# Kernel optimization log

Hardware: AMD Instinct MI355X
Metric: run time of the kernel (lower is better)

## Reference

```python
import jax, jax.numpy as jnp
import numpy as np

B, T, C, H = 4, 2048, 768, 12
HD = C // H  # 64
EPS = 1e-5


def layer_norm(x, g, b):
    mu = jnp.mean(x, axis=-1, keepdims=True)
    var = jnp.var(x, axis=-1, keepdims=True)
    return (x - mu) * jax.lax.rsqrt(var + EPS) * g + b


def setup_inputs() -> dict:
    key = jax.random.key(0)
    ks = jax.random.split(key, 14)
    s_c = 1.0 / np.sqrt(C)
    s_4c = 1.0 / np.sqrt(4 * C)
    return {
        "x": jax.random.normal(ks[0], (B, T, C), jnp.float32),
        # per-head Q/K/V projections stacked over heads [H, C, HD]
        "wq": jax.random.uniform(ks[1], (H, C, HD), jnp.float32, -s_c, s_c),
        "bq": jnp.zeros((H, HD), jnp.float32),
        "wk": jax.random.uniform(ks[2], (H, C, HD), jnp.float32, -s_c, s_c),
        "bk": jnp.zeros((H, HD), jnp.float32),
        "wv": jax.random.uniform(ks[3], (H, C, HD), jnp.float32, -s_c, s_c),
        "bv": jnp.zeros((H, HD), jnp.float32),
        "w_proj": jax.random.uniform(ks[4], (C, C), jnp.float32, -s_c, s_c),
        "b_proj": jnp.zeros((C,), jnp.float32),
        "w1": jax.random.uniform(ks[5], (C, 4 * C), jnp.float32, -s_c, s_c),
        "b1": jnp.zeros((4 * C,), jnp.float32),
        "w2": jax.random.uniform(ks[6], (4 * C, C), jnp.float32, -s_4c, s_4c),
        "b2": jnp.zeros((C,), jnp.float32),
        "g1": jnp.ones((C,), jnp.float32),
        "beta1": jnp.zeros((C,), jnp.float32),
        "g2": jnp.ones((C,), jnp.float32),
        "beta2": jnp.zeros((C,), jnp.float32),
    }


def reference(x, wq, bq, wk, bk, wv, bv, w_proj, b_proj, w1, b1, w2, b2, g1, beta1, g2, beta2):
    # --- attention sublayer ---
    h = layer_norm(x, g1, beta1)
    q = jnp.einsum('btc,hcd->bhtd', h, wq) + bq[None, :, None, :]
    k = jnp.einsum('btc,hcd->bhtd', h, wk) + bk[None, :, None, :]
    v = jnp.einsum('btc,hcd->bhtd', h, wv) + bv[None, :, None, :]
    # NOTE: source applies NO 1/sqrt(head_size) scaling
    scores = jnp.einsum('bhtd,bhsd->bhts', q, k)  # [B,H,T,T]
    causal = jnp.tril(jnp.ones((T, T), bool))
    scores = jnp.where(causal, scores, -jnp.inf)
    wei = jax.nn.softmax(scores, axis=-1)
    attn = jnp.einsum('bhts,bhsd->bhtd', wei, v)  # [B,H,T,HD]
    attn = attn.transpose(0, 2, 1, 3).reshape(B, T, C)  # concat heads
    x = x + attn @ w_proj + b_proj
    # --- MLP sublayer ---
    h2 = layer_norm(x, g2, beta2)
    x = x + jax.nn.relu(h2 @ w1 + b1) @ w2 + b2
    return x
```

## Files before the change

### kernel.cpp

```cpp
#include <hip/hip_runtime.h>
#include <hip/hip_bf16.h>
#include <math.h>

#define BB 4
#define TT 2048
#define CC 768
#define HH 12
#define HDIM 64
#define C4 3072
#define MM (BB*TT)
#define EPSL 1e-5f

typedef __bf16 bf16x8 __attribute__((ext_vector_type(8)));
typedef float f32x4 __attribute__((ext_vector_type(4)));

__device__ __forceinline__ ushort f2bf(float f) {
    union { float f; unsigned u; } v; v.f = f;
    unsigned r = v.u + 0x7fffu + ((v.u >> 16) & 1u);
    return (ushort)(r >> 16);
}

__device__ __forceinline__ void glds16(const void* g, void* l) {
    __builtin_amdgcn_global_load_lds(
        (const __attribute__((address_space(1))) void*)g,
        (__attribute__((address_space(3))) void*)l, 16, 0, 0);
}

__global__ __launch_bounds__(256) void ln_k(const float* __restrict__ X,
                                            const float* __restrict__ G,
                                            const float* __restrict__ Be,
                                            ushort* __restrict__ O)
{
    int row = blockIdx.x;
    const float* xr = X + (size_t)row * CC;
    int t = threadIdx.x;
    float v0 = xr[t], v1 = xr[t + 256], v2 = xr[t + 512];
    float s  = v0 + v1 + v2;
    float sq = v0*v0 + v1*v1 + v2*v2;
    #pragma unroll
    for (int off = 32; off; off >>= 1) {
        s  += __shfl_xor(s,  off);
        sq += __shfl_xor(sq, off);
    }
    __shared__ float red[8];
    int wv = t >> 6, ln = t & 63;
    if (ln == 0) { red[wv] = s; red[4 + wv] = sq; }
    __syncthreads();
    s  = red[0] + red[1] + red[2] + red[3];
    sq = red[4] + red[5] + red[6] + red[7];
    float mu  = s * (1.0f / CC);
    float var = sq * (1.0f / CC) - mu * mu;
    float rs  = rsqrtf(var + EPSL);
    ushort* orow = O + (size_t)row * CC;
    orow[t]       = f2bf((v0 - mu) * rs * G[t]       + Be[t]);
    orow[t + 256] = f2bf((v1 - mu) * rs * G[t + 256] + Be[t + 256]);
    orow[t + 512] = f2bf((v2 - mu) * rs * G[t + 512] + Be[t + 512]);
}

template<int MODE>
__global__ __launch_bounds__(256) void repack_k(const float* __restrict__ W,
                                                ushort* __restrict__ WT,
                                                int K, int N, int outStride)
{
    __shared__ float tl[64][65];
    int n0 = blockIdx.x * 64, k0 = blockIdx.y * 64;
    int c = threadIdx.x & 63, rr = threadIdx.x >> 6;
    #pragma unroll
    for (int i = 0; i < 16; ++i) {
        int r = i * 4 + rr;
        float v;
        if (MODE == 0) v = W[(size_t)(k0 + r) * N + n0 + c];
        else           v = W[((size_t)(n0 >> 6) * CC + k0 + r) * 64 + c];
        tl[r][c] = v;
    }
    __syncthreads();
    #pragma unroll
    for (int i = 0; i < 16; ++i) {
        int r = i * 4 + rr;
        WT[(size_t)(n0 + r) * outStride + k0 + c] = f2bf(tl[c][r]);
    }
}

template<int EPI>
__global__ __launch_bounds__(256) void gemm_bf16(
    const ushort* __restrict__ A, const ushort* __restrict__ BT,
    int M, int N, int K,
    void* __restrict__ ov0, void* __restrict__ ov1, void* __restrict__ ov2,
    const float* __restrict__ bias0, const float* __restrict__ bias1,
    const float* __restrict__ bias2,
    const float* __restrict__ resid, ushort* __restrict__ obf)
{
    __shared__ ushort Al[128 * 32];
    __shared__ ushort Bl[128 * 32];
    int bn = blockIdx.x, bm = blockIdx.y;
    int tid = threadIdx.x;
    int lane = tid & 63;
    int w = tid >> 6;
    int wr = (w >> 1) * 64, wc = (w & 1) * 64;
    int fr = lane & 15, kh = lane >> 4;

    f32x4 acc[4][4] = {};

    const size_t aRow = (size_t)bm * 128;
    const size_t bRow = (size_t)bn * 128;

    for (int k0 = 0; k0 < K; k0 += 32) {
        #pragma unroll
        for (int r = 0; r < 2; ++r) {
            int e = r * 256 + tid;
            glds16(A  + (aRow + (e >> 2)) * K + k0 + (e & 3) * 8, Al + e * 8);
            glds16(BT + (bRow + (e >> 2)) * K + k0 + (e & 3) * 8, Bl + e * 8);
        }
        __syncthreads();
        bf16x8 av[4], bv[4];
        #pragma unroll
        for (int i = 0; i < 4; ++i)
            av[i] = *(const bf16x8*)&Al[(wr + i * 16 + fr) * 32 + kh * 8];
        #pragma unroll
        for (int i = 0; i < 4; ++i)
            bv[i] = *(const bf16x8*)&Bl[(wc + i * 16 + fr) * 32 + kh * 8];
        #pragma unroll
        for (int i = 0; i < 4; ++i)
            #pragma unroll
            for (int j = 0; j < 4; ++j)
                acc[i][j] = __builtin_amdgcn_mfma_f32_16x16x32_bf16(av[i], bv[j], acc[i][j], 0, 0, 0);
        __syncthreads();
    }

    if (EPI == 1) {
        int seg = (bn * 128) / CC;
        ushort* op = (ushort*)(seg == 0 ? ov0 : (seg == 1 ? ov1 : ov2));
        const float* bsp = seg == 0 ? bias0 : (seg == 1 ? bias1 : bias2);
        int cb = bn * 128 - seg * CC + wc;
        int h = cb >> 6;
        #pragma unroll
        for (int i = 0; i < 4; ++i) {
            int row0 = bm * 128 + wr + i * 16 + kh * 4;
            int b = row0 >> 11;
            int t0 = row0 & (TT - 1);
            #pragma unroll
            for (int j = 0; j < 4; ++j) {
                int col = cb + j * 16 + fr;
                int d = col & 63;
                float bsv = bsp[col];
                #pragma unroll
                for (int r = 0; r < 4; ++r)
                    op[((size_t)(b * HH + h) * TT + t0 + r) * 64 + d] =
                        f2bf(acc[i][j][r] + bsv);
            }
        }
    } else if (EPI == 2) {
        float* o0 = (float*)ov0;
        int cb = bn * 128 + wc;
        #pragma unroll
        for (int i = 0; i < 4; ++i) {
            int row0 = bm * 128 + wr + i * 16 + kh * 4;
            #pragma unroll
            for (int j = 0; j < 4; ++j) {
                int col = cb + j * 16 + fr;
                float bsv = bias0[col];
                #pragma unroll
                for (int r = 0; r < 4; ++r) {
                    size_t idx = (size_t)(row0 + r) * N + col;
                    o0[idx] = acc[i][j][r] + bsv + resid[idx];
                }
            }
        }
    } else {
        int cb = bn * 128 + wc;
        #pragma unroll
        for (int i = 0; i < 4; ++i) {
            int row0 = bm * 128 + wr + i * 16 + kh * 4;
            #pragma unroll
            for (int j = 0; j < 4; ++j) {
                int col = cb + j * 16 + fr;
                float bsv = bias0[col];
                #pragma unroll
                for (int r = 0; r < 4; ++r) {
                    float v = fmaxf(acc[i][j][r] + bsv, 0.f);
                    obf[(size_t)(row0 + r) * N + col] = f2bf(v);
                }
            }
        }
    }
}

__global__ __launch_bounds__(256) void vtrans_k(const ushort* __restrict__ V,
                                                ushort* __restrict__ Vt)
{
    __shared__ ushort tl[64][72];
    int blk = blockIdx.x;
    int tt = blk & 31, bh = blk >> 5;
    size_t base = (size_t)bh * TT * 64;
    int t0 = tt * 64;
    int e = threadIdx.x;
    int rr = e >> 3, cc8 = (e & 7) * 8;
    #pragma unroll
    for (int p = 0; p < 2; ++p) {
        int t = p * 32 + rr;
        *(uint4*)&tl[t][cc8] = *(const uint4*)&V[base + (size_t)(t0 + t) * 64 + cc8];
    }
    __syncthreads();
    #pragma unroll
    for (int p = 0; p < 2; ++p) {
        int d = p * 32 + rr;
        ushort tmp[8];
        #pragma unroll
        for (int i = 0; i < 8; ++i) tmp[i] = tl[cc8 + i][d];
        *(uint4*)&Vt[base + (size_t)d * TT + t0 + cc8] = *(uint4*)tmp;
    }
}

__global__ __launch_bounds__(256) void attn_k(const ushort* __restrict__ Q,
                                              const ushort* __restrict__ Kb,
                                              const ushort* __restrict__ Vt,
                                              ushort* __restrict__ Ob)
{
    __shared__ ushort Kl[64][72];
    __shared__ ushort Vl[64][72];
    __shared__ ushort Pl[4][16][72];

    int blk = blockIdx.x;
    int pair = blk & 15;
    int bh = blk >> 4;
    int b = bh / HH, h = bh - b * HH;
    int tid = threadIdx.x, lane = tid & 63, w = tid >> 6;
    int c = lane & 15, g = lane >> 4;
    size_t base = (size_t)bh * TT * 64;
    int srow = tid >> 3, scol = (tid & 7) * 8;
    const float LOG2E = 1.44269504088896340736f;

    #pragma unroll
    for (int sel = 0; sel < 2; ++sel) {
        int qt = sel ? (31 - pair) : pair;
        int q0 = qt * 64;

        bf16x8 aq[2];
        #pragma unroll
        for (int kc = 0; kc < 2; ++kc) {
            bf16x8 raw = *(const bf16x8*)&Q[base + (size_t)(q0 + w * 16 + c) * 64 + kc * 32 + g * 8];
            #pragma unroll
            for (int e = 0; e < 8; ++e)
                raw[e] = (__bf16)((float)raw[e] * LOG2E);
            aq[kc] = raw;
        }

        f32x4 oa[4] = {};
        float mrun[4] = {-INFINITY, -INFINITY, -INFINITY, -INFINITY};
        float lrun[4] = {0.f, 0.f, 0.f, 0.f};

        for (int kv0 = 0; kv0 <= q0; kv0 += 64) {
            __syncthreads();
            #pragma unroll
            for (int p = 0; p < 2; ++p) {
                int r = p * 32 + srow;
                *(uint4*)&Kl[r][scol] = *(const uint4*)&Kb[base + (size_t)(kv0 + r) * 64 + scol];
                *(uint4*)&Vl[r][scol] = *(const uint4*)&Vt[base + (size_t)r * TT + kv0 + scol];
            }
            __syncthreads();

            f32x4 sa[4] = {};
            #pragma unroll
            for (int kc = 0; kc < 2; ++kc)
                #pragma unroll
                for (int j = 0; j < 4; ++j) {
                    bf16x8 kf = *(const bf16x8*)&Kl[j * 16 + c][kc * 32 + g * 8];
                    sa[j] = __builtin_amdgcn_mfma_f32_16x16x32_bf16(aq[kc], kf, sa[j], 0, 0, 0);
                }

            if (kv0 == q0) {
                #pragma unroll
                for (int j = 0; j < 4; ++j)
                    #pragma unroll
                    for (int r = 0; r < 4; ++r)
                        if (j * 16 + c > w * 16 + g * 4 + r) sa[j][r] = -1e30f;
            }

            float mx[4];
            #pragma unroll
            for (int r = 0; r < 4; ++r) {
                float m0 = fmaxf(fmaxf(sa[0][r], sa[1][r]), fmaxf(sa[2][r], sa[3][r]));
                #pragma unroll
                for (int off = 8; off; off >>= 1) m0 = fmaxf(m0, __shfl_xor(m0, off));
                mx[r] = m0;
            }
            float need = fmaxf(fmaxf(mx[0] - mrun[0], mx[1] - mrun[1]),
                               fmaxf(mx[2] - mrun[2], mx[3] - mrun[3]));
            if (!__all(need <= 11.5f)) {
                #pragma unroll
                for (int r = 0; r < 4; ++r) {
                    float mnew = fmaxf(mrun[r], mx[r]);
                    float sc = __builtin_amdgcn_exp2f(mrun[r] - mnew);
                    lrun[r] *= sc;
                    #pragma unroll
                    for (int j = 0; j < 4; ++j) oa[j][r] *= sc;
                    mrun[r] = mnew;
                }
            }
            #pragma unroll
            for (int r = 0; r < 4; ++r) {
                float ps = 0.f;
                #pragma unroll
                for (int j = 0; j < 4; ++j) {
                    float p = __builtin_amdgcn_exp2f(sa[j][r] - mrun[r]);
                    sa[j][r] = p;
                    ps += p;
                }
                lrun[r] += ps;
            }

            #pragma unroll
            for (int r = 0; r < 4; ++r)
                #pragma unroll
                for (int j = 0; j < 4; ++j)
                    Pl[w][g * 4 + r][j * 16 + c] = f2bf(sa[j][r]);

            bf16x8 pf[2];
            #pragma unroll
            for (int kc = 0; kc < 2; ++kc)
                pf[kc] = *(const bf16x8*)&Pl[w][c][kc * 32 + g * 8];

            #pragma unroll
            for (int kc = 0; kc < 2; ++kc)
                #pragma unroll
                for (int j = 0; j < 4; ++j) {
                    bf16x8 vf = *(const bf16x8*)&Vl[j * 16 + c][kc * 32 + g * 8];
                    oa[j] = __builtin_amdgcn_mfma_f32_16x16x32_bf16(pf[kc], vf, oa[j], 0, 0, 0);
                }
        }

        float inv[4];
        #pragma unroll
        for (int r = 0; r < 4; ++r) {
            float l = lrun[r];
            #pragma unroll
            for (int off = 8; off; off >>= 1) l += __shfl_xor(l, off);
            inv[r] = 1.0f / l;
        }
        size_t orow = (size_t)b * TT + q0 + w * 16;
        #pragma unroll
        for (int j = 0; j < 4; ++j)
            #pragma unroll
            for (int r = 0; r < 4; ++r) {
                float v = oa[j][r] * inv[r];
                Ob[(orow + g * 4 + r) * CC + h * 64 + j * 16 + c] = f2bf(v);
            }
    }
}

extern "C" void kernel_launch(void* const* d_in, const int* in_sizes, int n_in,
                              void* d_out, int out_size, void* d_ws, size_t ws_size,
                              hipStream_t stream)
{
    const float* x   = (const float*)d_in[0];
    const float* wq  = (const float*)d_in[1];
    const float* bq  = (const float*)d_in[2];
    const float* wk  = (const float*)d_in[3];
    const float* bk  = (const float*)d_in[4];
    const float* wvw = (const float*)d_in[5];
    const float* bv  = (const float*)d_in[6];
    const float* wp  = (const float*)d_in[7];
    const float* bp  = (const float*)d_in[8];
    const float* w1  = (const float*)d_in[9];
    const float* b1  = (const float*)d_in[10];
    const float* w2  = (const float*)d_in[11];
    const float* b2  = (const float*)d_in[12];
    const float* g1  = (const float*)d_in[13];
    const float* be1 = (const float*)d_in[14];
    const float* g2  = (const float*)d_in[15];
    const float* be2 = (const float*)d_in[16];

    float* out = (float*)d_out;
    const size_t S = (size_t)MM * CC;

    ushort* wsu   = (ushort*)d_ws;
    ushort* WTqkv = wsu;
    ushort* WTp   = WTqkv + (size_t)2304 * 768;
    ushort* WT1   = WTp   + (size_t)768 * 768;
    ushort* WT2   = WT1   + (size_t)3072 * 768;
    ushort* hbf   = WT2   + (size_t)768 * 3072;
    ushort* attnb = hbf   + S;
    ushort* qb    = attnb + S;
    ushort* kb    = qb + S;
    ushort* vb    = kb + S;
    ushort* vtb   = vb + S;
    ushort* midb  = qb;

    dim3 rg(12, 12);
    repack_k<1><<<rg, 256, 0, stream>>>(wq,  WTqkv,                      768, 768, 768);
    repack_k<1><<<rg, 256, 0, stream>>>(wk,  WTqkv + (size_t)768*768,    768, 768, 768);
    repack_k<1><<<rg, 256, 0, stream>>>(wvw, WTqkv + (size_t)2*768*768,  768, 768, 768);
    repack_k<0><<<rg, 256, 0, stream>>>(wp,  WTp, 768, 768, 768);
    repack_k<0><<<dim3(48, 12), 256, 0, stream>>>(w1, WT1, 768, 3072, 768);
    repack_k<0><<<dim3(12, 48), 256, 0, stream>>>(w2, WT2, 3072, 768, 3072);

    ln_k<<<MM, 256, 0, stream>>>(x, g1, be1, hbf);
    gemm_bf16<1><<<dim3(18, 64), 256, 0, stream>>>(hbf, WTqkv, MM, 2304, CC,
        qb, kb, vb, bq, bk, bv, nullptr, nullptr);
    vtrans_k<<<48 * 32, 256, 0, stream>>>(vb, vtb);
    attn_k<<<48 * 16, 256, 0, stream>>>(qb, kb, vtb, attnb);
    gemm_bf16<2><<<dim3(6, 64), 256, 0, stream>>>(attnb, WTp, MM, CC, CC,
        out, nullptr, nullptr, bp, nullptr, nullptr, x, nullptr);

    ln_k<<<MM, 256, 0, stream>>>(out, g2, be2, hbf);
    gemm_bf16<3><<<dim3(24, 64), 256, 0, stream>>>(hbf, WT1, MM, C4, CC,
        nullptr, nullptr, nullptr, b1, nullptr, nullptr, nullptr, midb);
    gemm_bf16<2><<<dim3(6, 64), 256, 0, stream>>>(midb, WT2, MM, CC, C4,
        out, nullptr, nullptr, b2, nullptr, nullptr, out, nullptr);
}
```

Before: 342.4 us.

## Swizzle block order for XCD locality and cheapen softmax rescale check

Remaps workgroup indices in the GEMM and attention kernels so that consecutive blocks landing on the same XCD share tiles or heads, aiming for better L2 reuse. In attention, the per-row max shuffle reduction now runs only when a lane-local max exceeds the smallest running max plus a threshold. This removes the shuffles from the common path, since the check is conservative. The bf16 conversion switches from manual rounding to the native cast, which may lower to a hardware convert. The attention swizzle hardcodes a stride of 96, which assumes a grid of 768 blocks.

```diff
diff --git a/kernel.cpp b/kernel.cpp
--- a/kernel.cpp
+++ b/kernel.cpp
@@ -92,7 +92,13 @@
 {
     __shared__ ushort Al[128 * 32];
     __shared__ ushort Bl[128 * 32];
-    int bn = blockIdx.x, bm = blockIdx.y;
+    int nbx = gridDim.x;
+    int nwg = nbx * gridDim.y;
+    int orig = blockIdx.y * nbx + blockIdx.x;
+    int swz = orig;
+    if ((nwg & 7) == 0) { int cpx = nwg >> 3; swz = (orig & 7) * cpx + (orig >> 3); }
+    int bn = swz % nbx, bm = swz / nbx;
+
     int tid = threadIdx.x;
     int lane = tid & 63;
     int w = tid >> 6;
@@ -220,9 +226,10 @@
     __shared__ ushort Vl[64][72];
     __shared__ ushort Pl[4][16][72];
 
-    int blk = blockIdx.x;
-    int pair = blk & 15;
-    int bh = blk >> 4;
+    int orig = blockIdx.x;
+    int swz = (orig & 7) * 96 + (orig >> 3);
+    int pair = swz & 15;
+    int bh = swz >> 4;
     int b = bh / HH, h = bh - b * HH;
     int tid = threadIdx.x, lane = tid & 63, w = tid >> 6;
     int c = lane & 15, g = lane >> 4;
@@ -276,20 +283,19 @@
                         if (j * 16 + c > w * 16 + g * 4 + r) sa[j][r] = -1e30f;
             }
 
-            float mx[4];
-            #pragma unroll
-            for (int r = 0; r < 4; ++r) {
-                float m0 = fmaxf(fmaxf(sa[0][r], sa[1][r]), fmaxf(sa[2][r], sa[3][r]));
-                #pragma unroll
-                for (int off = 8; off; off >>= 1) m0 = fmaxf(m0, __shfl_xor(m0, off));
-                mx[r] = m0;
-            }
-            float need = fmaxf(fmaxf(mx[0] - mrun[0], mx[1] - mrun[1]),
-                               fmaxf(mx[2] - mrun[2], mx[3] - mrun[3]));
-            if (!__all(need <= 11.5f)) {
+            float vlmax = sa[0][0];
+            #pragma unroll
+            for (int j = 0; j < 4; ++j)
+                #pragma unroll
+                for (int r = 0; r < 4; ++r) vlmax = fmaxf(vlmax, sa[j][r]);
+            float mmin = fminf(fminf(mrun[0], mrun[1]), fminf(mrun[2], mrun[3]));
+            if (!__all(vlmax <= mmin + 11.5f)) {
                 #pragma unroll
                 for (int r = 0; r < 4; ++r) {
-                    float mnew = fmaxf(mrun[r], mx[r]);
+                    float m0 = fmaxf(fmaxf(sa[0][r], sa[1][r]), fmaxf(sa[2][r], sa[3][r]));
+                    #pragma unroll
+                    for (int off = 8; off; off >>= 1) m0 = fmaxf(m0, __shfl_xor(m0, off));
+                    float mnew = fmaxf(mrun[r], m0);
                     float sc = __builtin_amdgcn_exp2f(mrun[r] - mnew);
                     lrun[r] *= sc;
                     #pragma unroll
@@ -313,7 +319,7 @@
             for (int r = 0; r < 4; ++r)
                 #pragma unroll
                 for (int j = 0; j < 4; ++j)
-                    Pl[w][g * 4 + r][j * 16 + c] = f2bf(sa[j][r]);
+                    Pl[w][g * 4 + r][j * 16 + c] = (ushort)__builtin_bit_cast(unsigned short, (__bf16)sa[j][r]);
 
             bf16x8 pf[2];
             #pragma unroll
```

Result: faster. 313.6 us (-8.4%).
